# Kernel tuning notes

Hardware: AMD Instinct MI355X
Metric: run time of the kernel (lower is better)

The kernel has to match this reference:

```python
import jax, jax.numpy as jnp
import numpy as np

def setup_inputs() -> dict:
    key = jax.random.key(0)
    QKV = jax.random.normal(key, (3, 2, 8, 4096, 64), dtype=jnp.float32)
    return {"QKV": QKV}

def reference(QKV):
    Q, K, V = QKV[0], QKV[1], QKV[2]            # each [B, H, N, d]
    scores = jnp.einsum('bhnd,bhmd->bhnm', Q, K)  # full N x N score matrix (no scaling, matching source)
    attn = jax.nn.softmax(scores, axis=-1)
    return jnp.einsum('bhnm,bhmd->bhnd', attn, V)
```

## Files before the change

### kernel.cpp

```cpp
#include <hip/hip_runtime.h>


typedef _Float16 f16x8 __attribute__((ext_vector_type(8)));
typedef _Float16 f16x2 __attribute__((ext_vector_type(2)));
typedef short s16x8 __attribute__((ext_vector_type(8)));
typedef short s16x4 __attribute__((ext_vector_type(4)));
typedef float f32x4 __attribute__((ext_vector_type(4)));
typedef unsigned u32x4 __attribute__((ext_vector_type(4)));

#define NHEADS 16
#define SEQ 4096
#define HDIM 64
#define BR 128
#define NH 2
#define BC 64
#define KP 72

__device__ __forceinline__ float fast_exp2(float x) {
#if __has_builtin(__builtin_amdgcn_exp2f)
  return __builtin_amdgcn_exp2f(x);
#else
  return exp2f(x);
#endif
}

__device__ __forceinline__ f16x2 pkrtz(float a, float b) {
  return __builtin_bit_cast(f16x2, __builtin_amdgcn_cvt_pkrtz(a, b));
}

__device__ __forceinline__ unsigned short f2bf(float f) {
  unsigned u = __builtin_bit_cast(unsigned, f);
  u += 0x7fffu + ((u >> 16) & 1u);
  return (unsigned short)(u >> 16);
}

__device__ __forceinline__ unsigned bfpack2(float a, float b) {
#if __has_builtin(__builtin_amdgcn_perm)
  return __builtin_amdgcn_perm(__builtin_bit_cast(unsigned, b),
                               __builtin_bit_cast(unsigned, a), 0x07060302u);
#else
  return (__builtin_bit_cast(unsigned, b) & 0xffff0000u) |
         (__builtin_bit_cast(unsigned, a) >> 16);
#endif
}

__device__ __forceinline__ void gload16(const void* g, void* l) {
  __builtin_amdgcn_global_load_lds(
      (const __attribute__((address_space(1))) unsigned int*)g,
      (__attribute__((address_space(3))) unsigned int*)l, 16, 0, 0);
}

__global__ __launch_bounds__(256) void prep(const float* __restrict__ QKV,
                                            _Float16* __restrict__ K16,
                                            short* __restrict__ Vt) {
  const size_t tensElems = (size_t)NHEADS * SEQ * HDIM;
  __shared__ __align__(16) short T[64 * KP];
  if (blockIdx.x < 2048) {
    const float* Kf = QKV + tensElems;
    size_t i = ((size_t)blockIdx.x * 256 + threadIdx.x) * 8;
    float4 a = *(const float4*)(Kf + i);
    float4 b = *(const float4*)(Kf + i + 4);
    union { f16x8 v; f16x2 h2[4]; } u;
    u.h2[0] = pkrtz(a.x, a.y);
    u.h2[1] = pkrtz(a.z, a.w);
    u.h2[2] = pkrtz(b.x, b.y);
    u.h2[3] = pkrtz(b.z, b.w);
    size_t r = (i >> 6) & 63, c = (i >> 3) & 7;
    size_t dst = (i >> 12) * 4096 + r * 64 + (((c + r) & 7) << 3);
    *(f16x8*)(K16 + dst) = u.v;
  } else {
    const int vb = blockIdx.x - 2048;
    const int bh = vb >> 6;
    const int nt = vb & 63;
    const float* Vh = QKV + 2 * tensElems + (size_t)bh * SEQ * HDIM +
                      (size_t)nt * 64 * HDIM;
    const int t = threadIdx.x;
    #pragma unroll
    for (int p = 0; p < 4; ++p) {
      int idx = t + p * 256;
      int row = idx >> 4, c4 = (idx & 15) << 2;
      float4 v = *(const float4*)(Vh + row * HDIM + c4);
      s16x4 h;
      h[0] = (short)f2bf(v.x); h[1] = (short)f2bf(v.y);
      h[2] = (short)f2bf(v.z); h[3] = (short)f2bf(v.w);
      *(s16x4*)&T[row * KP + c4] = h;
    }
    __syncthreads();
    short* outT = Vt + ((size_t)bh * 64 + nt) * 4096;
    const int p0 = 2 * t;
    const int d0 = p0 >> 3;
    const int k0 = (((p0 & 7) - d0) & 7) << 3;
    const int k1 = ((((p0 + 1) & 7) - d0) & 7) << 3;
    s16x8 o0, o1;
    #pragma unroll
    for (int j = 0; j < 8; ++j) o0[j] = T[(k0 + j) * KP + d0];
    #pragma unroll
    for (int j = 0; j < 8; ++j) o1[j] = T[(k1 + j) * KP + d0];
    *(s16x8*)(outT + p0 * 8) = o0;
    *(s16x8*)(outT + p0 * 8 + 8) = o1;
  }
}

template <bool PRE>
__global__ __launch_bounds__(256, 2) void flash_attn(const float* __restrict__ QKV,
                                                     const _Float16* __restrict__ K16g,
                                                     const short* __restrict__ Vt16,
                                                     float* __restrict__ Out) {
  const size_t headElems = (size_t)SEQ * HDIM;
  const size_t tensElems = (size_t)NHEADS * headElems;
  const int bh = blockIdx.x & 15;
  const int qt = blockIdx.x >> 4;
  const int ktN = SEQ / BC;

  const float* Q = QKV + (size_t)bh * headElems;
  const float* Kf = QKV + tensElems + (size_t)bh * headElems;
  const float* Vf = QKV + 2 * tensElems + (size_t)bh * headElems;
  const _Float16* Kg16 = K16g + (size_t)bh * headElems;
  const short* Vg16 = Vt16 + (size_t)bh * headElems;
  float* O = Out + (size_t)bh * headElems;

  const int tid = threadIdx.x;
  const int wave = tid >> 6;
  const int lane = tid & 63;
  const int g = lane >> 4;
  const int l16 = lane & 15;

  __shared__ __align__(16) _Float16 KsB[2][64 * 64];
  __shared__ __align__(16) short VsB[2][64 * 64];

  const float LOG2E = 1.4426950408889634f;
  const int qbase = qt * BR + wave * (16 * NH);
  f16x8 qf[NH][2];
  #pragma unroll
  for (int h = 0; h < NH; ++h) {
    const float* qp = Q + (size_t)(qbase + h * 16 + l16) * HDIM + g * 8;
    #pragma unroll
    for (int c = 0; c < 2; ++c) {
      float4 a = *(const float4*)(qp + c * 32);
      float4 b = *(const float4*)(qp + c * 32 + 4);
      union { f16x8 v; f16x2 h2[4]; } u;
      u.h2[0] = pkrtz(a.x * LOG2E, a.y * LOG2E);
      u.h2[1] = pkrtz(a.z * LOG2E, a.w * LOG2E);
      u.h2[2] = pkrtz(b.x * LOG2E, b.y * LOG2E);
      u.h2[3] = pkrtz(b.z * LOG2E, b.w * LOG2E);
      qf[h][c] = u.v;
    }
  }

  s16x8 onesb;
  #pragma unroll
  for (int j = 0; j < 8; ++j) onesb[j] = (short)0x3F80;

  const int rbase = 8 * (l16 >> 2) + 4 * (l16 & 1) + ((l16 >> 1) & 1);
  const int so = tid << 4;

  auto stage = [&](int buf, int kt) {
    if constexpr (PRE) {
      const char* kg = (const char*)Kg16 + (size_t)kt * 8192 + so;
      const char* vg = (const char*)Vg16 + (size_t)kt * 8192 + so;
      char* kl = (char*)&KsB[buf][0] + (wave << 10);
      char* vl = (char*)&VsB[buf][0] + (wave << 10);
      gload16(kg, kl);
      gload16(kg + 4096, kl + 4096);
      gload16(vg, vl);
      gload16(vg + 4096, vl + 4096);
    } else {
      _Float16* Kd = KsB[buf];
      short* Vd = VsB[buf];
      const int sr = tid >> 2;
      const int s = tid & 3;
      const float* kg = Kf + (size_t)(kt * BC + sr) * HDIM + s * 16;
      float4 a = *(const float4*)(kg), b = *(const float4*)(kg + 4);
      float4 c = *(const float4*)(kg + 8), d = *(const float4*)(kg + 12);
      union { f16x8 v; f16x2 h2[4]; } ka, kb;
      ka.h2[0] = pkrtz(a.x, a.y);
      ka.h2[1] = pkrtz(a.z, a.w);
      ka.h2[2] = pkrtz(b.x, b.y);
      ka.h2[3] = pkrtz(b.z, b.w);
      kb.h2[0] = pkrtz(c.x, c.y);
      kb.h2[1] = pkrtz(c.z, c.w);
      kb.h2[2] = pkrtz(d.x, d.y);
      kb.h2[3] = pkrtz(d.z, d.w);
      *(f16x8*)&Kd[sr * 64 + (((2 * s + sr) & 7) << 3)] = ka.v;
      *(f16x8*)&Kd[sr * 64 + (((2 * s + 1 + sr) & 7) << 3)] = kb.v;
      const float* vg = Vf + (size_t)(kt * BC + sr) * HDIM + s * 16;
      float4 va = *(const float4*)(vg), vb = *(const float4*)(vg + 4);
      float4 vc = *(const float4*)(vg + 8), vd = *(const float4*)(vg + 12);
      float vv[16] = {va.x, va.y, va.z, va.w, vb.x, vb.y, vb.z, vb.w,
                      vc.x, vc.y, vc.z, vc.w, vd.x, vd.y, vd.z, vd.w};
      #pragma unroll
      for (int j = 0; j < 16; ++j) {
        int dd = s * 16 + j;
        Vd[dd * 64 + ((((sr >> 3) + dd) & 7) << 3) + (sr & 7)] =
            (short)f2bf(vv[j]);
      }
    }
  };

  f32x4 acc[NH][4];
  f32x4 acc_l[NH];
  #pragma unroll
  for (int h = 0; h < NH; ++h) {
    #pragma unroll
    for (int nt = 0; nt < 4; ++nt)
      #pragma unroll
      for (int i = 0; i < 4; ++i) acc[h][nt][i] = 0.f;
    #pragma unroll
    for (int i = 0; i < 4; ++i) acc_l[h][i] = 0.f;
  }

  stage(0, 0);
  int cur = 0;

  for (int it = 0; it < ktN; ++it) {
    __syncthreads();
    if (it + 1 < ktN) stage(cur ^ 1, it + 1);
    const _Float16* Kb = KsB[cur];
    const short* Vb = VsB[cur];

    #pragma unroll
    for (int hh = 0; hh < 2; ++hh) {
      const int half = hh ^ (wave & 1);
      u32x4 Wp[NH];
      #pragma unroll
      for (int jt2 = 0; jt2 < 2; ++jt2) {
        const int r = rbase + (half << 5) + (jt2 << 1);
        const int ka = r * 64 + (((g + r) & 7) << 3);
        f16x8 k0 = *(const f16x8*)&Kb[ka];
        f16x8 k1 = *(const f16x8*)&Kb[ka ^ 32];
        #pragma unroll
        for (int h = 0; h < NH; ++h) {
          f32x4 z;
          z[0] = z[1] = z[2] = z[3] = 0.f;
          z = __builtin_amdgcn_mfma_f32_16x16x32_f16(k0, qf[h][0], z, 0, 0, 0);
          z = __builtin_amdgcn_mfma_f32_16x16x32_f16(k1, qf[h][1], z, 0, 0, 0);
          float p0 = fast_exp2(z[0]);
          float p1 = fast_exp2(z[1]);
          float p2 = fast_exp2(z[2]);
          float p3 = fast_exp2(z[3]);
          Wp[h][jt2] = bfpack2(p0, p2);
          Wp[h][jt2 + 2] = bfpack2(p1, p3);
        }
      }
      __builtin_amdgcn_s_setprio(1);
      #pragma unroll
      for (int h = 0; h < NH; ++h) {
        acc_l[h] = __builtin_amdgcn_mfma_f32_16x16x32_bf16(
            __builtin_bit_cast(s16x8, Wp[h]), onesb, acc_l[h], 0, 0, 0);
      }
      #pragma unroll
      for (int nt = 0; nt < 4; ++nt) {
        const int row = nt * 16 + l16;
        int va = row * 64 + (((g + row) & 7) << 3);
        if (half) va ^= 32;
        s16x8 v = *(const s16x8*)&Vb[va];
        #pragma unroll
        for (int h = 0; h < NH; ++h) {
          acc[h][nt] = __builtin_amdgcn_mfma_f32_16x16x32_bf16(
              __builtin_bit_cast(s16x8, Wp[h]), v, acc[h][nt], 0, 0, 0);
        }
      }
      __builtin_amdgcn_s_setprio(0);
    }

    cur ^= 1;
  }

  #pragma unroll
  for (int h = 0; h < NH; ++h) {
    #pragma unroll
    for (int ri = 0; ri < 4; ++ri) {
      float lB = 1.0f / acc_l[h][ri];
      const int row = qbase + h * 16 + 4 * g + ri;
      #pragma unroll
      for (int nt = 0; nt < 4; ++nt)
        O[(size_t)row * HDIM + nt * 16 + l16] = acc[h][nt][ri] * lB;
    }
  }
}

extern "C" void kernel_launch(void* const* d_in, const int* in_sizes, int n_in,
                              void* d_out, int out_size, void* d_ws, size_t ws_size,
                              hipStream_t stream) {
  const float* QKV = (const float*)d_in[0];
  float* Out = (float*)d_out;
  const size_t tensElems = (size_t)NHEADS * SEQ * HDIM;
  const size_t k16Bytes = tensElems * sizeof(_Float16);
  const size_t vtBytes = tensElems * sizeof(short);

  dim3 block(256);

  if (ws_size >= k16Bytes + vtBytes) {
    _Float16* K16 = (_Float16*)d_ws;
    short* Vt16 = (short*)((char*)d_ws + k16Bytes);
    hipLaunchKernelGGL(prep, dim3(3072), block, 0, stream, QKV, K16, Vt16);
    hipLaunchKernelGGL((flash_attn<true>), dim3(NHEADS * (SEQ / BR)), block, 0,
                       stream, QKV, K16, Vt16, Out);
  } else {
    hipLaunchKernelGGL((flash_attn<false>), dim3(NHEADS * (SEQ / BR)), block, 0,
                       stream, QKV, (const _Float16*)nullptr,
                       (const short*)nullptr, Out);
  }
}
```

Before: 157.0 us.

## Shrink query tile to 64 rows with one 16-row block per wave

Reduces the query tile from 128 to 64 rows so each wave processes a single 16-row block instead of two. It also drops the per-wave swap of which key half is processed first. This doubles the number of workgroups and lowers register pressure, aiming for more parallelism and occupancy. The cost is that each K/V tile staged in shared memory is reused by half as many query rows, so global and LDS traffic per unit of compute doubles.

```diff
diff --git a/kernel.cpp b/kernel.cpp
--- a/kernel.cpp
+++ b/kernel.cpp
@@ -11,8 +11,8 @@
 #define NHEADS 16
 #define SEQ 4096
 #define HDIM 64
-#define BR 128
-#define NH 2
+#define BR 64
+#define NH 1
 #define BC 64
 #define KP 72
 
@@ -129,11 +129,10 @@
   __shared__ __align__(16) short VsB[2][64 * 64];
 
   const float LOG2E = 1.4426950408889634f;
-  const int qbase = qt * BR + wave * (16 * NH);
-  f16x8 qf[NH][2];
-  #pragma unroll
-  for (int h = 0; h < NH; ++h) {
-    const float* qp = Q + (size_t)(qbase + h * 16 + l16) * HDIM + g * 8;
+  const int qbase = qt * BR + wave * 16;
+  f16x8 qf[2];
+  {
+    const float* qp = Q + (size_t)(qbase + l16) * HDIM + g * 8;
     #pragma unroll
     for (int c = 0; c < 2; ++c) {
       float4 a = *(const float4*)(qp + c * 32);
@@ -143,7 +142,7 @@
       u.h2[1] = pkrtz(a.z * LOG2E, a.w * LOG2E);
       u.h2[2] = pkrtz(b.x * LOG2E, b.y * LOG2E);
       u.h2[3] = pkrtz(b.z * LOG2E, b.w * LOG2E);
-      qf[h][c] = u.v;
+      qf[c] = u.v;
     }
   }
 
@@ -197,17 +196,14 @@
     }
   };
 
-  f32x4 acc[NH][4];
-  f32x4 acc_l[NH];
-  #pragma unroll
-  for (int h = 0; h < NH; ++h) {
-    #pragma unroll
-    for (int nt = 0; nt < 4; ++nt)
-      #pragma unroll
-      for (int i = 0; i < 4; ++i) acc[h][nt][i] = 0.f;
-    #pragma unroll
-    for (int i = 0; i < 4; ++i) acc_l[h][i] = 0.f;
-  }
+  f32x4 acc[4];
+  f32x4 acc_l;
+  #pragma unroll
+  for (int nt = 0; nt < 4; ++nt)
+    #pragma unroll
+    for (int i = 0; i < 4; ++i) acc[nt][i] = 0.f;
+  #pragma unroll
+  for (int i = 0; i < 4; ++i) acc_l[i] = 0.f;
 
   stage(0, 0);
   int cur = 0;
@@ -219,46 +215,36 @@
     const short* Vb = VsB[cur];
 
     #pragma unroll
-    for (int hh = 0; hh < 2; ++hh) {
-      const int half = hh ^ (wave & 1);
-      u32x4 Wp[NH];
+    for (int half = 0; half < 2; ++half) {
+      u32x4 Wp;
       #pragma unroll
       for (int jt2 = 0; jt2 < 2; ++jt2) {
         const int r = rbase + (half << 5) + (jt2 << 1);
         const int ka = r * 64 + (((g + r) & 7) << 3);
         f16x8 k0 = *(const f16x8*)&Kb[ka];
         f16x8 k1 = *(const f16x8*)&Kb[ka ^ 32];
-        #pragma unroll
-        for (int h = 0; h < NH; ++h) {
-          f32x4 z;
-          z[0] = z[1] = z[2] = z[3] = 0.f;
-          z = __builtin_amdgcn_mfma_f32_16x16x32_f16(k0, qf[h][0], z, 0, 0, 0);
-          z = __builtin_amdgcn_mfma_f32_16x16x32_f16(k1, qf[h][1], z, 0, 0, 0);
-          float p0 = fast_exp2(z[0]);
-          float p1 = fast_exp2(z[1]);
-          float p2 = fast_exp2(z[2]);
-          float p3 = fast_exp2(z[3]);
-          Wp[h][jt2] = bfpack2(p0, p2);
-          Wp[h][jt2 + 2] = bfpack2(p1, p3);
-        }
+        f32x4 z;
+        z[0] = z[1] = z[2] = z[3] = 0.f;
+        z = __builtin_amdgcn_mfma_f32_16x16x32_f16(k0, qf[0], z, 0, 0, 0);
+        z = __builtin_amdgcn_mfma_f32_16x16x32_f16(k1, qf[1], z, 0, 0, 0);
+        float p0 = fast_exp2(z[0]);
+        float p1 = fast_exp2(z[1]);
+        float p2 = fast_exp2(z[2]);
+        float p3 = fast_exp2(z[3]);
+        Wp[jt2] = bfpack2(p0, p2);
+        Wp[jt2 + 2] = bfpack2(p1, p3);
       }
       __builtin_amdgcn_s_setprio(1);
-      #pragma unroll
-      for (int h = 0; h < NH; ++h) {
-        acc_l[h] = __builtin_amdgcn_mfma_f32_16x16x32_bf16(
-            __builtin_bit_cast(s16x8, Wp[h]), onesb, acc_l[h], 0, 0, 0);
-      }
+      acc_l = __builtin_amdgcn_mfma_f32_16x16x32_bf16(
+          __builtin_bit_cast(s16x8, Wp), onesb, acc_l, 0, 0, 0);
       #pragma unroll
       for (int nt = 0; nt < 4; ++nt) {
         const int row = nt * 16 + l16;
         int va = row * 64 + (((g + row) & 7) << 3);
         if (half) va ^= 32;
         s16x8 v = *(const s16x8*)&Vb[va];
-        #pragma unroll
-        for (int h = 0; h < NH; ++h) {
-          acc[h][nt] = __builtin_amdgcn_mfma_f32_16x16x32_bf16(
-              __builtin_bit_cast(s16x8, Wp[h]), v, acc[h][nt], 0, 0, 0);
-        }
+        acc[nt] = __builtin_amdgcn_mfma_f32_16x16x32_bf16(
+            __builtin_bit_cast(s16x8, Wp), v, acc[nt], 0, 0, 0);
       }
       __builtin_amdgcn_s_setprio(0);
     }
@@ -267,15 +253,12 @@
   }
 
   #pragma unroll
-  for (int h = 0; h < NH; ++h) {
-    #pragma unroll
-    for (int ri = 0; ri < 4; ++ri) {
-      float lB = 1.0f / acc_l[h][ri];
-      const int row = qbase + h * 16 + 4 * g + ri;
-      #pragma unroll
-      for (int nt = 0; nt < 4; ++nt)
-        O[(size_t)row * HDIM + nt * 16 + l16] = acc[h][nt][ri] * lB;
-    }
+  for (int ri = 0; ri < 4; ++ri) {
+    float lB = 1.0f / acc_l[ri];
+    const int row = qbase + 4 * g + ri;
+    #pragma unroll
+    for (int nt = 0; nt < 4; ++nt)
+      O[(size_t)row * HDIM + nt * 16 + l16] = acc[nt][ri] * lB;
   }
 }
 
```

New measurement: 169.9 us. 1.08x slower.

## Software-pipeline QK of next tile with PV of previous tile using triple V buffer

Applied to the files above, without the earlier changes.

Restructures the main loop so the QK^T MFMA and exp for tile n+1 are issued alongside the PV MFMAs for tile n, using two register sets of probabilities and a third V shared-memory buffer. The aim is to overlap the exp/transcendental work with matrix-core work and to hide LDS latency across tiles. It also drops the per-wave half-order swizzle. In exchange it raises register pressure (two probability arrays) and uses more LDS, which may lower occupancy.

```diff
diff --git a/kernel.cpp b/kernel.cpp
--- a/kernel.cpp
+++ b/kernel.cpp
@@ -126,7 +126,7 @@
   const int l16 = lane & 15;
 
   __shared__ __align__(16) _Float16 KsB[2][64 * 64];
-  __shared__ __align__(16) short VsB[2][64 * 64];
+  __shared__ __align__(16) short VsB[3][64 * 64];
 
   const float LOG2E = 1.4426950408889634f;
   const int qbase = qt * BR + wave * (16 * NH);
@@ -154,22 +154,22 @@
   const int rbase = 8 * (l16 >> 2) + 4 * (l16 & 1) + ((l16 >> 1) & 1);
   const int so = tid << 4;
 
-  auto stage = [&](int buf, int kt) {
+  auto stage = [&](int n) {
     if constexpr (PRE) {
-      const char* kg = (const char*)Kg16 + (size_t)kt * 8192 + so;
-      const char* vg = (const char*)Vg16 + (size_t)kt * 8192 + so;
-      char* kl = (char*)&KsB[buf][0] + (wave << 10);
-      char* vl = (char*)&VsB[buf][0] + (wave << 10);
+      const char* kg = (const char*)Kg16 + (size_t)n * 8192 + so;
+      const char* vg = (const char*)Vg16 + (size_t)n * 8192 + so;
+      char* kl = (char*)&KsB[n & 1][0] + (wave << 10);
+      char* vl = (char*)&VsB[n % 3][0] + (wave << 10);
       gload16(kg, kl);
       gload16(kg + 4096, kl + 4096);
       gload16(vg, vl);
       gload16(vg + 4096, vl + 4096);
     } else {
-      _Float16* Kd = KsB[buf];
-      short* Vd = VsB[buf];
+      _Float16* Kd = KsB[n & 1];
+      short* Vd = VsB[n % 3];
       const int sr = tid >> 2;
       const int s = tid & 3;
-      const float* kg = Kf + (size_t)(kt * BC + sr) * HDIM + s * 16;
+      const float* kg = Kf + (size_t)(n * BC + sr) * HDIM + s * 16;
       float4 a = *(const float4*)(kg), b = *(const float4*)(kg + 4);
       float4 c = *(const float4*)(kg + 8), d = *(const float4*)(kg + 12);
       union { f16x8 v; f16x2 h2[4]; } ka, kb;
@@ -183,7 +183,7 @@
       kb.h2[3] = pkrtz(d.z, d.w);
       *(f16x8*)&Kd[sr * 64 + (((2 * s + sr) & 7) << 3)] = ka.v;
       *(f16x8*)&Kd[sr * 64 + (((2 * s + 1 + sr) & 7) << 3)] = kb.v;
-      const float* vg = Vf + (size_t)(kt * BC + sr) * HDIM + s * 16;
+      const float* vg = Vf + (size_t)(n * BC + sr) * HDIM + s * 16;
       float4 va = *(const float4*)(vg), vb = *(const float4*)(vg + 4);
       float4 vc = *(const float4*)(vg + 8), vd = *(const float4*)(vg + 12);
       float vv[16] = {va.x, va.y, va.z, va.w, vb.x, vb.y, vb.z, vb.w,
@@ -209,19 +209,10 @@
     for (int i = 0; i < 4; ++i) acc_l[h][i] = 0.f;
   }
 
-  stage(0, 0);
-  int cur = 0;
-
-  for (int it = 0; it < ktN; ++it) {
-    __syncthreads();
-    if (it + 1 < ktN) stage(cur ^ 1, it + 1);
-    const _Float16* Kb = KsB[cur];
-    const short* Vb = VsB[cur];
-
-    #pragma unroll
-    for (int hh = 0; hh < 2; ++hh) {
-      const int half = hh ^ (wave & 1);
-      u32x4 Wp[NH];
+  auto qk = [&](int n, u32x4 (&W)[NH][2]) {
+    const _Float16* Kb = &KsB[n & 1][0];
+    #pragma unroll
+    for (int half = 0; half < 2; ++half) {
       #pragma unroll
       for (int jt2 = 0; jt2 < 2; ++jt2) {
         const int r = rbase + (half << 5) + (jt2 << 1);
@@ -238,15 +229,22 @@
           float p1 = fast_exp2(z[1]);
           float p2 = fast_exp2(z[2]);
           float p3 = fast_exp2(z[3]);
-          Wp[h][jt2] = bfpack2(p0, p2);
-          Wp[h][jt2 + 2] = bfpack2(p1, p3);
+          W[h][half][jt2] = bfpack2(p0, p2);
+          W[h][half][jt2 + 2] = bfpack2(p1, p3);
         }
       }
-      __builtin_amdgcn_s_setprio(1);
+    }
+  };
+
+  auto pv = [&](int n, u32x4 (&W)[NH][2]) {
+    const short* Vb = &VsB[n % 3][0];
+    __builtin_amdgcn_s_setprio(1);
+    #pragma unroll
+    for (int half = 0; half < 2; ++half) {
       #pragma unroll
       for (int h = 0; h < NH; ++h) {
         acc_l[h] = __builtin_amdgcn_mfma_f32_16x16x32_bf16(
-            __builtin_bit_cast(s16x8, Wp[h]), onesb, acc_l[h], 0, 0, 0);
+            __builtin_bit_cast(s16x8, W[h][half]), onesb, acc_l[h], 0, 0, 0);
       }
       #pragma unroll
       for (int nt = 0; nt < 4; ++nt) {
@@ -257,14 +255,35 @@
         #pragma unroll
         for (int h = 0; h < NH; ++h) {
           acc[h][nt] = __builtin_amdgcn_mfma_f32_16x16x32_bf16(
-              __builtin_bit_cast(s16x8, Wp[h]), v, acc[h][nt], 0, 0, 0);
+              __builtin_bit_cast(s16x8, W[h][half]), v, acc[h][nt], 0, 0, 0);
         }
       }
-      __builtin_amdgcn_s_setprio(0);
-    }
-
-    cur ^= 1;
-  }
+    }
+    __builtin_amdgcn_s_setprio(0);
+  };
+
+  u32x4 WA[NH][2], WB[NH][2];
+
+  stage(0);
+  __syncthreads();
+  stage(1);
+  qk(0, WA);
+
+  for (int m = 0; m < (ktN - 2) / 2; ++m) {
+    const int n1 = 2 * m + 1;
+    __syncthreads();
+    stage(n1 + 1);
+    qk(n1, WB);
+    pv(n1 - 1, WA);
+    __syncthreads();
+    if (n1 + 2 < ktN) stage(n1 + 2);
+    qk(n1 + 1, WA);
+    pv(n1, WB);
+  }
+  __syncthreads();
+  qk(ktN - 1, WB);
+  pv(ktN - 2, WA);
+  pv(ktN - 1, WB);
 
   #pragma unroll
   for (int h = 0; h < NH; ++h) {
```

Result: faster. 152.9 us (-2.6%).

## Stage two K/V tiles per barrier using a four-slot LDS ring

Applied to the files above, without the earlier changes.

Grows the K/V shared-memory ring from two to four slots. Each loop iteration now stages two tiles ahead and computes two tiles, so the kernel hits half as many __syncthreads barriers and keeps more loads in flight. The cost is twice the LDS footprint (64 KB instead of 32 KB), which may lower occupancy. It also relies on the tile count being even.

```diff
diff --git a/kernel.cpp b/kernel.cpp
--- a/kernel.cpp
+++ b/kernel.cpp
@@ -125,8 +125,8 @@
   const int g = lane >> 4;
   const int l16 = lane & 15;
 
-  __shared__ __align__(16) _Float16 KsB[2][64 * 64];
-  __shared__ __align__(16) short VsB[2][64 * 64];
+  __shared__ __align__(16) _Float16 KsB[4][64 * 64];
+  __shared__ __align__(16) short VsB[4][64 * 64];
 
   const float LOG2E = 1.4426950408889634f;
   const int qbase = qt * BR + wave * (16 * NH);
@@ -154,22 +154,22 @@
   const int rbase = 8 * (l16 >> 2) + 4 * (l16 & 1) + ((l16 >> 1) & 1);
   const int so = tid << 4;
 
-  auto stage = [&](int buf, int kt) {
+  auto stage = [&](int n) {
     if constexpr (PRE) {
-      const char* kg = (const char*)Kg16 + (size_t)kt * 8192 + so;
-      const char* vg = (const char*)Vg16 + (size_t)kt * 8192 + so;
-      char* kl = (char*)&KsB[buf][0] + (wave << 10);
-      char* vl = (char*)&VsB[buf][0] + (wave << 10);
+      const char* kg = (const char*)Kg16 + (size_t)n * 8192 + so;
+      const char* vg = (const char*)Vg16 + (size_t)n * 8192 + so;
+      char* kl = (char*)&KsB[n & 3][0] + (wave << 10);
+      char* vl = (char*)&VsB[n & 3][0] + (wave << 10);
       gload16(kg, kl);
       gload16(kg + 4096, kl + 4096);
       gload16(vg, vl);
       gload16(vg + 4096, vl + 4096);
     } else {
-      _Float16* Kd = KsB[buf];
-      short* Vd = VsB[buf];
+      _Float16* Kd = KsB[n & 3];
+      short* Vd = VsB[n & 3];
       const int sr = tid >> 2;
       const int s = tid & 3;
-      const float* kg = Kf + (size_t)(kt * BC + sr) * HDIM + s * 16;
+      const float* kg = Kf + (size_t)(n * BC + sr) * HDIM + s * 16;
       float4 a = *(const float4*)(kg), b = *(const float4*)(kg + 4);
       float4 c = *(const float4*)(kg + 8), d = *(const float4*)(kg + 12);
       union { f16x8 v; f16x2 h2[4]; } ka, kb;
@@ -183,7 +183,7 @@
       kb.h2[3] = pkrtz(d.z, d.w);
       *(f16x8*)&Kd[sr * 64 + (((2 * s + sr) & 7) << 3)] = ka.v;
       *(f16x8*)&Kd[sr * 64 + (((2 * s + 1 + sr) & 7) << 3)] = kb.v;
-      const float* vg = Vf + (size_t)(kt * BC + sr) * HDIM + s * 16;
+      const float* vg = Vf + (size_t)(n * BC + sr) * HDIM + s * 16;
       float4 va = *(const float4*)(vg), vb = *(const float4*)(vg + 4);
       float4 vc = *(const float4*)(vg + 8), vd = *(const float4*)(vg + 12);
       float vv[16] = {va.x, va.y, va.z, va.w, vb.x, vb.y, vb.z, vb.w,
@@ -209,15 +209,9 @@
     for (int i = 0; i < 4; ++i) acc_l[h][i] = 0.f;
   }
 
-  stage(0, 0);
-  int cur = 0;
-
-  for (int it = 0; it < ktN; ++it) {
-    __syncthreads();
-    if (it + 1 < ktN) stage(cur ^ 1, it + 1);
-    const _Float16* Kb = KsB[cur];
-    const short* Vb = VsB[cur];
-
+  auto compute = [&](int n) {
+    const _Float16* Kb = &KsB[n & 3][0];
+    const short* Vb = &VsB[n & 3][0];
     #pragma unroll
     for (int hh = 0; hh < 2; ++hh) {
       const int half = hh ^ (wave & 1);
@@ -262,8 +256,19 @@
       }
       __builtin_amdgcn_s_setprio(0);
     }
-
-    cur ^= 1;
+  };
+
+  stage(0);
+  stage(1);
+
+  for (int m = 0; m < ktN / 2; ++m) {
+    __syncthreads();
+    if (2 * m + 3 < ktN) {
+      stage(2 * m + 2);
+      stage(2 * m + 3);
+    }
+    compute(2 * m);
+    compute(2 * m + 1);
   }
 
   #pragma unroll
```

After: 159.4 us. About the same (+1.5%).
